# Kernel tuning notes

Measured on AMD Instinct MI355X. Metric: run time of the kernel, lower is better.

The kernel has to match this reference:

```python
import jax, jax.numpy as jnp
import numpy as np

FG_THRESH = 0.5  # fg_iou_thresh in RetinaNetLoss.__init__
BG_THRESH = 0.4  # bg_iou_thresh
BELOW_LOW_QUALITY = -1
BETWEEN_THRESHOLDS = -2


def _make_boxes(key, lead_shape, img_size=800.0, max_wh=128.0):
    # Build valid xyxy boxes (x1<x2, y1<y2) inside an img_size image.
    k1, k2 = jax.random.split(key)
    cxcy = jax.random.uniform(k1, lead_shape + (2,), minval=0.0, maxval=img_size)
    wh = jax.random.uniform(k2, lead_shape + (2,), minval=8.0, maxval=max_wh)
    return jnp.concatenate([cxcy - wh * 0.5, cxcy + wh * 0.5], axis=-1)


def setup_inputs() -> dict:
    key = jax.random.key(0)
    kb, ka = jax.random.split(key)
    B, G, A = 8, 64, 120000
    gt_boxes = _make_boxes(kb, (B, G))                 # [B, G, 4] per-image gt boxes
    anchors = _make_boxes(ka, (A,), max_wh=256.0)      # [A, 4] shared anchors
    return {"gt_boxes": gt_boxes, "anchors": anchors}


def _box_iou(boxes1, boxes2):
    # boxes1 [G,4], boxes2 [A,4] -> IoU [G,A] (torchvision box_ops.box_iou)
    area1 = (boxes1[:, 2] - boxes1[:, 0]) * (boxes1[:, 3] - boxes1[:, 1])  # [G]
    area2 = (boxes2[:, 2] - boxes2[:, 0]) * (boxes2[:, 3] - boxes2[:, 1])  # [A]
    lt = jnp.maximum(boxes1[:, None, :2], boxes2[None, :, :2])  # [G,A,2]
    rb = jnp.minimum(boxes1[:, None, 2:], boxes2[None, :, 2:])  # [G,A,2]
    wh = jnp.clip(rb - lt, 0.0)
    inter = wh[..., 0] * wh[..., 1]  # [G,A]
    return inter / (area1[:, None] + area2[None, :] - inter)


def _match(quality):
    # torchvision Matcher(0.5, 0.4, allow_low_quality_matches=True) on quality [G,A]
    matched_vals = quality.max(axis=0)                      # [A] best IoU per anchor
    all_matches = jnp.argmax(quality, axis=0)               # [A] pre-threshold matches
    matches = jnp.where(matched_vals < BG_THRESH, BELOW_LOW_QUALITY, all_matches)
    matches = jnp.where((matched_vals >= BG_THRESH) & (matched_vals < FG_THRESH),
                        BETWEEN_THRESHOLDS, matches)
    # low-quality match recovery: anchors achieving the per-gt max keep their match
    highest_per_gt = quality.max(axis=1, keepdims=True)     # [G,1]
    pred_update = (quality == highest_per_gt).any(axis=0)   # [A]
    matches = jnp.where(pred_update, all_matches, matches)
    return matches.astype(jnp.int64), matched_vals


def reference(gt_boxes, anchors):
    # gt_boxes [B,G,4], anchors [A,4] -> matched_idxs [B,A] int64, matched_vals [B,A]
    def per_image(boxes):
        return _match(_box_iou(boxes, anchors))
    matched_idxs, matched_vals = jax.vmap(per_image)(gt_boxes)
    return matched_idxs, matched_vals
```

## Files before the change

### kernel.cpp

```cpp
#include <hip/hip_runtime.h>


static constexpr int G = 64;
static constexpr int NCELL = 256;

__device__ __forceinline__ float opaque(float x) {
    asm volatile("" : "+v"(x));
    return x;
}

__device__ __forceinline__ int vindex(int i) {
    asm volatile("" : "+v"(i));
    return i;
}

__device__ __forceinline__ float box_area(float x1, float y1, float x2, float y2) {
    return opaque(__fmul_rn(__fsub_rn(x2, x1), __fsub_rn(y2, y1)));
}

__device__ __forceinline__ float inter_area(float gx1, float gy1, float gx2, float gy2,
                                            float ax1, float ay1, float ax2, float ay2) {
    float ltx = fmaxf(gx1, ax1);
    float lty = fmaxf(gy1, ay1);
    float rbx = fminf(gx2, ax2);
    float rby = fminf(gy2, ay2);
    float w = fmaxf(__fsub_rn(rbx, ltx), 0.0f);
    float h = fmaxf(__fsub_rn(rby, lty), 0.0f);
    return opaque(__fmul_rn(w, h));
}

__device__ __forceinline__ float div_rn(float n, float d) {
    float r = __builtin_amdgcn_rcpf(d);
    float e = fmaf(-d, r, 1.0f);
    r = fmaf(e, r, r);
    float q = __fmul_rn(n, r);
    float s = fmaf(-d, q, n);
    q = fmaf(s, r, q);
    s = fmaf(-d, q, n);
    q = fmaf(s, r, q);
    return q;
}

#define DPP_MAX_STAGE(x, ctrl)                                                   \
    do {                                                                         \
        int _yi = __builtin_amdgcn_update_dpp(__float_as_int(x),                 \
                                              __float_as_int(x), (ctrl),         \
                                              0xf, 0xf, false);                  \
        (x) = fmaxf((x), __int_as_float(_yi));                                   \
    } while (0)

#define DPP_MIN_STAGE(x, ctrl)                                                   \
    do {                                                                         \
        int _yi = __builtin_amdgcn_update_dpp(__float_as_int(x),                 \
                                              __float_as_int(x), (ctrl),         \
                                              0xf, 0xf, false);                  \
        (x) = fminf((x), __int_as_float(_yi));                                   \
    } while (0)

__device__ __forceinline__ float wave_max_lane63(float x) {
    DPP_MAX_STAGE(x, 0xB1);
    DPP_MAX_STAGE(x, 0x4E);
    DPP_MAX_STAGE(x, 0x141);
    DPP_MAX_STAGE(x, 0x140);
    DPP_MAX_STAGE(x, 0x142);
    DPP_MAX_STAGE(x, 0x143);
    return x;
}

__device__ __forceinline__ float wave_min_lane63(float x) {
    DPP_MIN_STAGE(x, 0xB1);
    DPP_MIN_STAGE(x, 0x4E);
    DPP_MIN_STAGE(x, 0x141);
    DPP_MIN_STAGE(x, 0x140);
    DPP_MIN_STAGE(x, 0x142);
    DPP_MIN_STAGE(x, 0x143);
    return x;
}

__device__ __forceinline__ float lane63_bcast(float x) {
    return __int_as_float(__builtin_amdgcn_readlane(__float_as_int(x), 63));
}

__device__ __forceinline__ int cell_of(float4 ab) {
    float cx = (ab.x + ab.z) * 0.5f;
    float cy = (ab.y + ab.w) * 0.5f;
    int cxi = (int)(cx * 0.02f); cxi = cxi < 0 ? 0 : (cxi > 15 ? 15 : cxi);
    int cyi = (int)(cy * 0.02f); cyi = cyi < 0 ? 0 : (cyi > 15 ? 15 : cyi);
    return cyi * 16 + cxi;
}

__global__ void k_count(const float* __restrict__ gt,
                        const float* __restrict__ anchors,
                        unsigned int* __restrict__ bh,
                        unsigned int* __restrict__ hpg,
                        float* __restrict__ gab,
                        int A, int NB, int BG) {
    int t = threadIdx.x;
    int gi = blockIdx.x * 256 + t;
    if (gi < BG) {
        hpg[gi] = 0u;
        float4 gb = ((const float4*)gt)[gi];
        gab[gi] = box_area(gb.x, gb.y, gb.z, gb.w);
    }
    __shared__ unsigned int h[NCELL];
    h[t] = 0u;
    __syncthreads();
    int a = blockIdx.x * 256 + t;
    if (a < A) atomicAdd(&h[cell_of(((const float4*)anchors)[a])], 1u);
    __syncthreads();
    bh[(size_t)t * NB + blockIdx.x] = h[t];
}

__global__ void k_rowscan(unsigned int* __restrict__ bh,
                          unsigned int* __restrict__ cellTot, int NB) {
    const int c = blockIdx.x;
    unsigned int* row = bh + (size_t)c * NB;
    __shared__ unsigned int s[256];
    __shared__ unsigned int carry;
    if (threadIdx.x == 0) carry = 0u;
    __syncthreads();
    for (int base = 0; base < NB; base += 256) {
        int i = base + threadIdx.x;
        unsigned int v = (i < NB) ? row[i] : 0u;
        s[threadIdx.x] = v;
        __syncthreads();
        for (int d = 1; d < 256; d <<= 1) {
            unsigned int add = (threadIdx.x >= d) ? s[threadIdx.x - d] : 0u;
            __syncthreads();
            s[threadIdx.x] += add;
            __syncthreads();
        }
        unsigned int excl = s[threadIdx.x] - v + carry;
        if (i < NB) row[i] = excl;
        __syncthreads();
        if (threadIdx.x == 255) carry += s[255];
        __syncthreads();
    }
    if (threadIdx.x == 0) cellTot[c] = carry;
}

__global__ void k_scat(const float* __restrict__ anchors,
                       const unsigned int* __restrict__ bh,
                       const unsigned int* __restrict__ cellTot,
                       float* __restrict__ sortedA,
                       int* __restrict__ orig, int A, int NB) {
    __shared__ unsigned int cb[NCELL];
    __shared__ unsigned int tot[NCELL];
    __shared__ unsigned int h[NCELL];
    int t = threadIdx.x;
    unsigned int v = cellTot[t];
    cb[t] = v;
    tot[t] = v;
    h[t] = 0u;
    __syncthreads();
    for (int d = 1; d < NCELL; d <<= 1) {
        unsigned int add = (t >= d) ? cb[t - d] : 0u;
        __syncthreads();
        cb[t] += add;
        __syncthreads();
    }
    int a = blockIdx.x * 256 + t;
    if (a < A) {
        float4 ab = ((const float4*)anchors)[a];
        int c = cell_of(ab);
        unsigned int lr = atomicAdd(&h[c], 1u);
        unsigned int base = cb[c] - tot[c];
        unsigned int pos = base + bh[(size_t)c * NB + blockIdx.x] + lr;
        ((float4*)sortedA)[pos] = ab;
        orig[pos] = a;
    }
}

template <bool SCATTER>
__global__ __launch_bounds__(256, 4)
void pass1_k(const float* __restrict__ gt,
             const float* __restrict__ anchors,
             const float* __restrict__ gab,
             unsigned int* __restrict__ hpg,
             unsigned int* __restrict__ sredg,
             int* __restrict__ amaxS,
             const int* __restrict__ orig,
             float2* __restrict__ outiv,
             int A, int nchunks) {
    const int b = blockIdx.y;
    const int t = threadIdx.x;

    __shared__ unsigned int sred[G];
    if (t < G) sred[t] = 0u;
    __syncthreads();

    const int base = blockIdx.x * 1024;
    float ax1[4], ay1[4], ax2[4], ay2[4], aar[4];
    bool val[4];
#pragma unroll
    for (int k = 0; k < 4; ++k) {
        int a = base + k * 256 + t;
        val[k] = (a < A);
        float4 ab = ((const float4*)anchors)[val[k] ? a : 0];
        ax1[k] = val[k] ? ab.x : 3.0e38f;
        ay1[k] = val[k] ? ab.y : 3.0e38f;
        ax2[k] = val[k] ? ab.z : -3.0e38f;
        ay2[k] = val[k] ? ab.w : -3.0e38f;
        aar[k] = val[k] ? box_area(ax1[k], ay1[k], ax2[k], ay2[k]) : 0.0f;
    }

    float wx1 = fminf(fminf(ax1[0], ax1[1]), fminf(ax1[2], ax1[3]));
    float wy1 = fminf(fminf(ay1[0], ay1[1]), fminf(ay1[2], ay1[3]));
    float wx2 = fmaxf(fmaxf(ax2[0], ax2[1]), fmaxf(ax2[2], ax2[3]));
    float wy2 = fmaxf(fmaxf(ay2[0], ay2[1]), fmaxf(ay2[2], ay2[3]));
    wx1 = lane63_bcast(wave_min_lane63(wx1));
    wy1 = lane63_bcast(wave_min_lane63(wy1));
    wx2 = lane63_bcast(wave_max_lane63(wx2));
    wy2 = lane63_bcast(wave_max_lane63(wy2));

    const float4* gtb = (const float4*)gt + (size_t)b * G;
    const float* gas = gab + b * G;

    float vmax[4] = {0.0f, 0.0f, 0.0f, 0.0f};
    int amax[4] = {0, 0, 0, 0};

#pragma unroll 4
    for (int g = 0; g < G; ++g) {
        const int gv = vindex(g);
        const float4 gb = gtb[gv];
        float tlx = fmaxf(gb.x, wx1), trx = fminf(gb.z, wx2);
        float tly = fmaxf(gb.y, wy1), tby = fminf(gb.w, wy2);
        if ((trx > tlx) && (tby > tly)) {
            float inter[4];
#pragma unroll
            for (int k = 0; k < 4; ++k)
                inter[k] = inter_area(gb.x, gb.y, gb.z, gb.w,
                                      ax1[k], ay1[k], ax2[k], ay2[k]);
            float itest = fmaxf(fmaxf(inter[0], inter[1]),
                                fmaxf(inter[2], inter[3]));
            if (__any(itest > 0.0f)) {
                const float ga = gas[gv];
                float m = 0.0f;
#pragma unroll
                for (int k = 0; k < 4; ++k) {
                    float denom = __fsub_rn(__fadd_rn(ga, aar[k]), inter[k]);
                    float q = div_rn(inter[k], denom);
                    if (q > vmax[k]) { vmax[k] = q; amax[k] = g; }
                    m = fmaxf(m, q);
                }
                m = wave_max_lane63(m);
                if ((t & 63) == 63)
                    atomicMax(&sred[g], __float_as_uint(m));
            }
        }
    }

#pragma unroll
    for (int k = 0; k < 4; ++k) {
        if (!val[k]) continue;
        int a = base + k * 256 + t;
        size_t sidx = (size_t)b * A + a;
        amaxS[sidx] = amax[k];
        int mt;
        if (vmax[k] < 0.4f) mt = -1;
        else if (vmax[k] < 0.5f) mt = -2;
        else mt = amax[k];
        int ao = SCATTER ? orig[a] : a;
        outiv[(size_t)b * A + ao] = make_float2((float)mt, vmax[k]);
    }

    __syncthreads();
    if (t < G) {
        atomicMax(&hpg[b * G + t], sred[t]);
        sredg[(size_t)(b * nchunks + blockIdx.x) * G + t] = sred[t];
    }
}

template <bool SCATTER>
__global__ __launch_bounds__(256, 8)
void k_patch(const float* __restrict__ gt,
             const float* __restrict__ anchors,
             const float* __restrict__ gab,
             const unsigned int* __restrict__ hpg,
             const unsigned int* __restrict__ sredg,
             const int* __restrict__ amaxS,
             const int* __restrict__ orig,
             float2* __restrict__ outiv,
             int A, int nchunks) {
    const int b = blockIdx.y;
    const int t = threadIdx.x;
    const int base = blockIdx.x * 1024;

    const unsigned int* sb = sredg + (size_t)(b * nchunks + blockIdx.x) * G;
    const unsigned int* hb = hpg + b * G;

    unsigned long long E = 0ull;
#pragma unroll 16
    for (int g = 0; g < G; ++g)
        E |= (sb[g] == hb[g]) ? (1ull << g) : 0ull;
    if (E == 0ull) return;

    const float4* gtb = (const float4*)gt + (size_t)b * G;
    const float* gas = gab + b * G;
    float ax1[4], ay1[4], ax2[4], ay2[4], aar[4];
    bool val[4];
#pragma unroll
    for (int k = 0; k < 4; ++k) {
        int a = base + k * 256 + t;
        val[k] = (a < A);
        float4 ab = ((const float4*)anchors)[val[k] ? a : 0];
        ax1[k] = val[k] ? ab.x : 3.0e38f;
        ay1[k] = val[k] ? ab.y : 3.0e38f;
        ax2[k] = val[k] ? ab.z : -3.0e38f;
        ay2[k] = val[k] ? ab.w : -3.0e38f;
        aar[k] = val[k] ? box_area(ax1[k], ay1[k], ax2[k], ay2[k]) : 0.0f;
    }

    bool pu[4] = {false, false, false, false};
    unsigned long long e = E;
    while (e) {
        int g = __builtin_ctzll(e);
        e &= e - 1;
        float4 gb = gtb[g];
        float ga = gas[g];
        float hgf = __uint_as_float(hb[g]);
#pragma unroll
        for (int k = 0; k < 4; ++k) {
            float inter = inter_area(gb.x, gb.y, gb.z, gb.w,
                                     ax1[k], ay1[k], ax2[k], ay2[k]);
            float denom = __fsub_rn(__fadd_rn(ga, aar[k]), inter);
            float q = div_rn(inter, denom);
            pu[k] = pu[k] | (q == hgf);
        }
    }

#pragma unroll
    for (int k = 0; k < 4; ++k) {
        int a = base + k * 256 + t;
        if (!val[k] || !pu[k]) continue;
        int ao = SCATTER ? orig[a] : a;
        outiv[(size_t)b * A + ao].x = (float)amaxS[(size_t)b * A + a];
    }
}

__global__ __launch_bounds__(256, 8)
void k_emit(const float2* __restrict__ outiv,
            float* __restrict__ out_idx,
            float* __restrict__ out_val,
            int A) {
    const int b = blockIdx.y;
    const int base = blockIdx.x * 1024;
#pragma unroll
    for (int k = 0; k < 4; ++k) {
        int a = base + k * 256 + threadIdx.x;
        if (a >= A) continue;
        size_t i = (size_t)b * A + a;
        float2 v = outiv[i];
        out_idx[i] = v.x;
        out_val[i] = v.y;
    }
}

extern "C" void kernel_launch(void* const* d_in, const int* in_sizes, int n_in,
                              void* d_out, int out_size, void* d_ws, size_t ws_size,
                              hipStream_t stream) {
    const float* gt = (const float*)d_in[0];
    const float* anchors = (const float*)d_in[1];
    const int BG = in_sizes[0] / 4;
    const int B = BG / G;
    const int A = in_sizes[1] / 4;

    const int nchunks = (A + 1023) / 1024;
    const int NB = (A + 255) / 256;

    unsigned int* ws = (unsigned int*)d_ws;
    unsigned int* hpg = ws;
    float* gab = (float*)(ws + 512);
    unsigned int* cellTot = ws + 1024;
    unsigned int* bh = ws + 1280;
    size_t soff = 1280 + (size_t)NB * 256;
    soff = (soff + 3) & ~(size_t)3;
    float* sortedA = (float*)(ws + soff);
    int* orig = (int*)(ws + soff + 4 * (size_t)A);
    unsigned int* sredg = ws + soff + 5 * (size_t)A;
    size_t ooff = soff + 5 * (size_t)A + (size_t)nchunks * B * G;
    ooff = (ooff + 1) & ~(size_t)1;
    float2* outiv = (float2*)(ws + ooff);
    int* amaxS = (int*)(ws + ooff + 2 * (size_t)B * A);
    const size_t need = (ooff + 3 * (size_t)B * A) * 4;
    const bool sorted = (ws_size >= need);

    float* out_idx = (float*)d_out;
    float* out_val = out_idx + (size_t)B * A;

    dim3 g1(nchunks, B);
    if (sorted) {
        k_count<<<NB, 256, 0, stream>>>(gt, anchors, bh, hpg, gab, A, NB, BG);
        k_rowscan<<<NCELL, 256, 0, stream>>>(bh, cellTot, NB);
        k_scat<<<NB, 256, 0, stream>>>(anchors, bh, cellTot, sortedA, orig, A, NB);
        pass1_k<true><<<g1, 256, 0, stream>>>(gt, sortedA, gab, hpg, sredg,
                                              amaxS, orig, outiv, A, nchunks);
        k_patch<true><<<g1, 256, 0, stream>>>(gt, sortedA, gab, hpg, sredg,
                                              amaxS, orig, outiv, A, nchunks);
        k_emit<<<g1, 256, 0, stream>>>(outiv, out_idx, out_val, A);
    } else {
        k_count<<<NB, 256, 0, stream>>>(gt, anchors, bh, hpg, gab, A, NB, BG);
        pass1_k<false><<<g1, 256, 0, stream>>>(gt, anchors, gab, hpg, sredg,
                                               amaxS, orig, outiv, A, nchunks);
        k_patch<false><<<g1, 256, 0, stream>>>(gt, anchors, gab, hpg, sredg,
                                               amaxS, orig, outiv, A, nchunks);
        k_emit<<<g1, 256, 0, stream>>>(outiv, out_idx, out_val, A);
    }
}
```

Baseline: 67.81 us.

## Process all images per anchor thread and store intermediates anchor-major

The first pass now gives each thread one anchor and loops over all eight images' GT boxes, instead of four anchors per thread for a single image. This reuses anchor loads and wave bounding windows across images and uses 256-anchor chunks, so the GT-window culling is finer. The intermediate outiv/amaxS buffers become anchor-major [A,B], and the patch and emit kernels are reindexed to match. Risks are less per-thread ILP, a longer serial loop per thread, and strided writes in the patch kernel. B is also hardcoded to 8.

New measurement: 135.2 us. +99.3%, slower.

```diff
diff --git a/kernel.cpp b/kernel.cpp
--- a/kernel.cpp
+++ b/kernel.cpp
@@ -2,6 +2,7 @@
 
 
 static constexpr int G = 64;
+static constexpr int B = 8;
 static constexpr int NCELL = 256;
 
 __device__ __forceinline__ float opaque(float x) {
@@ -181,94 +182,80 @@
              int* __restrict__ amaxS,
              const int* __restrict__ orig,
              float2* __restrict__ outiv,
-             int A, int nchunks) {
-    const int b = blockIdx.y;
+             int A) {
     const int t = threadIdx.x;
 
-    __shared__ unsigned int sred[G];
-    if (t < G) sred[t] = 0u;
-    __syncthreads();
-
-    const int base = blockIdx.x * 1024;
-    float ax1[4], ay1[4], ax2[4], ay2[4], aar[4];
-    bool val[4];
+    __shared__ unsigned int sred[B * G];
+    sred[t] = 0u;
+    sred[t + 256] = 0u;
+    __syncthreads();
+
+    const int a = blockIdx.x * 256 + t;
+    const bool v = (a < A);
+    float4 ab = ((const float4*)anchors)[v ? a : 0];
+    float ax1 = v ? ab.x : 3.0e38f;
+    float ay1 = v ? ab.y : 3.0e38f;
+    float ax2 = v ? ab.z : -3.0e38f;
+    float ay2 = v ? ab.w : -3.0e38f;
+    float aar = v ? box_area(ax1, ay1, ax2, ay2) : 0.0f;
+
+    float wx1 = lane63_bcast(wave_min_lane63(ax1));
+    float wy1 = lane63_bcast(wave_min_lane63(ay1));
+    float wx2 = lane63_bcast(wave_max_lane63(ax2));
+    float wy2 = lane63_bcast(wave_max_lane63(ay2));
+
+    const float4* gtb = (const float4*)gt;
+    const float* gas = gab;
+
+    float vmax[B];
+    int amax[B];
 #pragma unroll
-    for (int k = 0; k < 4; ++k) {
-        int a = base + k * 256 + t;
-        val[k] = (a < A);
-        float4 ab = ((const float4*)anchors)[val[k] ? a : 0];
-        ax1[k] = val[k] ? ab.x : 3.0e38f;
-        ay1[k] = val[k] ? ab.y : 3.0e38f;
-        ax2[k] = val[k] ? ab.z : -3.0e38f;
-        ay2[k] = val[k] ? ab.w : -3.0e38f;
-        aar[k] = val[k] ? box_area(ax1[k], ay1[k], ax2[k], ay2[k]) : 0.0f;
-    }
-
-    float wx1 = fminf(fminf(ax1[0], ax1[1]), fminf(ax1[2], ax1[3]));
-    float wy1 = fminf(fminf(ay1[0], ay1[1]), fminf(ay1[2], ay1[3]));
-    float wx2 = fmaxf(fmaxf(ax2[0], ax2[1]), fmaxf(ax2[2], ax2[3]));
-    float wy2 = fmaxf(fmaxf(ay2[0], ay2[1]), fmaxf(ay2[2], ay2[3]));
-    wx1 = lane63_bcast(wave_min_lane63(wx1));
-    wy1 = lane63_bcast(wave_min_lane63(wy1));
-    wx2 = lane63_bcast(wave_max_lane63(wx2));
-    wy2 = lane63_bcast(wave_max_lane63(wy2));
-
-    const float4* gtb = (const float4*)gt + (size_t)b * G;
-    const float* gas = gab + b * G;
-
-    float vmax[4] = {0.0f, 0.0f, 0.0f, 0.0f};
-    int amax[4] = {0, 0, 0, 0};
-
+    for (int b = 0; b < B; ++b) { vmax[b] = 0.0f; amax[b] = 0; }
+
+#pragma unroll
+    for (int b = 0; b < B; ++b) {
 #pragma unroll 4
-    for (int g = 0; g < G; ++g) {
-        const int gv = vindex(g);
-        const float4 gb = gtb[gv];
-        float tlx = fmaxf(gb.x, wx1), trx = fminf(gb.z, wx2);
-        float tly = fmaxf(gb.y, wy1), tby = fminf(gb.w, wy2);
-        if ((trx > tlx) && (tby > tly)) {
-            float inter[4];
-#pragma unroll
-            for (int k = 0; k < 4; ++k)
-                inter[k] = inter_area(gb.x, gb.y, gb.z, gb.w,
-                                      ax1[k], ay1[k], ax2[k], ay2[k]);
-            float itest = fmaxf(fmaxf(inter[0], inter[1]),
-                                fmaxf(inter[2], inter[3]));
-            if (__any(itest > 0.0f)) {
-                const float ga = gas[gv];
-                float m = 0.0f;
-#pragma unroll
-                for (int k = 0; k < 4; ++k) {
-                    float denom = __fsub_rn(__fadd_rn(ga, aar[k]), inter[k]);
-                    float q = div_rn(inter[k], denom);
-                    if (q > vmax[k]) { vmax[k] = q; amax[k] = g; }
-                    m = fmaxf(m, q);
+        for (int g = 0; g < G; ++g) {
+            const int gv = vindex(b * G + g);
+            const float4 gb = gtb[gv];
+            float tlx = fmaxf(gb.x, wx1), trx = fminf(gb.z, wx2);
+            float tly = fmaxf(gb.y, wy1), tby = fminf(gb.w, wy2);
+            if ((trx > tlx) && (tby > tly)) {
+                float inter = inter_area(gb.x, gb.y, gb.z, gb.w,
+                                         ax1, ay1, ax2, ay2);
+                if (__any(inter > 0.0f)) {
+                    const float ga = gas[gv];
+                    float denom = __fsub_rn(__fadd_rn(ga, aar), inter);
+                    float q = div_rn(inter, denom);
+                    if (q > vmax[b]) { vmax[b] = q; amax[b] = g; }
+                    float m = wave_max_lane63(q);
+                    if ((t & 63) == 63)
+                        atomicMax(&sred[b * G + g], __float_as_uint(m));
                 }
-                m = wave_max_lane63(m);
-                if ((t & 63) == 63)
-                    atomicMax(&sred[g], __float_as_uint(m));
             }
         }
     }
 
+    if (v) {
+        int ao = SCATTER ? orig[a] : a;
+        float2* ov = outiv + (size_t)ao * B;
+        int* am = amaxS + (size_t)a * B;
 #pragma unroll
-    for (int k = 0; k < 4; ++k) {
-        if (!val[k]) continue;
-        int a = base + k * 256 + t;
-        size_t sidx = (size_t)b * A + a;
-        amaxS[sidx] = amax[k];
-        int mt;
-        if (vmax[k] < 0.4f) mt = -1;
-        else if (vmax[k] < 0.5f) mt = -2;
-        else mt = amax[k];
-        int ao = SCATTER ? orig[a] : a;
-        outiv[(size_t)b * A + ao] = make_float2((float)mt, vmax[k]);
-    }
-
-    __syncthreads();
-    if (t < G) {
-        atomicMax(&hpg[b * G + t], sred[t]);
-        sredg[(size_t)(b * nchunks + blockIdx.x) * G + t] = sred[t];
-    }
+        for (int b = 0; b < B; ++b) {
+            am[b] = amax[b];
+            int mt;
+            if (vmax[b] < 0.4f) mt = -1;
+            else if (vmax[b] < 0.5f) mt = -2;
+            else mt = amax[b];
+            ov[b] = make_float2((float)mt, vmax[b]);
+        }
+    }
+
+    __syncthreads();
+    atomicMax(&hpg[t], sred[t]);
+    atomicMax(&hpg[t + 256], sred[t + 256]);
+    sredg[(size_t)blockIdx.x * 512 + t] = sred[t];
+    sredg[(size_t)blockIdx.x * 512 + t + 256] = sred[t + 256];
 }
 
 template <bool SCATTER>
@@ -281,12 +268,11 @@
              const int* __restrict__ amaxS,
              const int* __restrict__ orig,
              float2* __restrict__ outiv,
-             int A, int nchunks) {
+             int A) {
     const int b = blockIdx.y;
     const int t = threadIdx.x;
-    const int base = blockIdx.x * 1024;
-
-    const unsigned int* sb = sredg + (size_t)(b * nchunks + blockIdx.x) * G;
+
+    const unsigned int* sb = sredg + (size_t)blockIdx.x * 512 + b * G;
     const unsigned int* hb = hpg + b * G;
 
     unsigned long long E = 0ull;
@@ -295,23 +281,19 @@
         E |= (sb[g] == hb[g]) ? (1ull << g) : 0ull;
     if (E == 0ull) return;
 
+    const int a = blockIdx.x * 256 + t;
+    const bool v = (a < A);
+    float4 ab = ((const float4*)anchors)[v ? a : 0];
+    float ax1 = v ? ab.x : 3.0e38f;
+    float ay1 = v ? ab.y : 3.0e38f;
+    float ax2 = v ? ab.z : -3.0e38f;
+    float ay2 = v ? ab.w : -3.0e38f;
+    float aar = v ? box_area(ax1, ay1, ax2, ay2) : 0.0f;
+
     const float4* gtb = (const float4*)gt + (size_t)b * G;
     const float* gas = gab + b * G;
-    float ax1[4], ay1[4], ax2[4], ay2[4], aar[4];
-    bool val[4];
-#pragma unroll
-    for (int k = 0; k < 4; ++k) {
-        int a = base + k * 256 + t;
-        val[k] = (a < A);
-        float4 ab = ((const float4*)anchors)[val[k] ? a : 0];
-        ax1[k] = val[k] ? ab.x : 3.0e38f;
-        ay1[k] = val[k] ? ab.y : 3.0e38f;
-        ax2[k] = val[k] ? ab.z : -3.0e38f;
-        ay2[k] = val[k] ? ab.w : -3.0e38f;
-        aar[k] = val[k] ? box_area(ax1[k], ay1[k], ax2[k], ay2[k]) : 0.0f;
-    }
-
-    bool pu[4] = {false, false, false, false};
+
+    bool pu = false;
     unsigned long long e = E;
     while (e) {
         int g = __builtin_ctzll(e);
@@ -319,22 +301,15 @@
         float4 gb = gtb[g];
         float ga = gas[g];
         float hgf = __uint_as_float(hb[g]);
-#pragma unroll
-        for (int k = 0; k < 4; ++k) {
-            float inter = inter_area(gb.x, gb.y, gb.z, gb.w,
-                                     ax1[k], ay1[k], ax2[k], ay2[k]);
-            float denom = __fsub_rn(__fadd_rn(ga, aar[k]), inter);
-            float q = div_rn(inter, denom);
-            pu[k] = pu[k] | (q == hgf);
-        }
-    }
-
-#pragma unroll
-    for (int k = 0; k < 4; ++k) {
-        int a = base + k * 256 + t;
-        if (!val[k] || !pu[k]) continue;
+        float inter = inter_area(gb.x, gb.y, gb.z, gb.w, ax1, ay1, ax2, ay2);
+        float denom = __fsub_rn(__fadd_rn(ga, aar), inter);
+        float q = div_rn(inter, denom);
+        pu = pu | (q == hgf);
+    }
+
+    if (v && pu) {
         int ao = SCATTER ? orig[a] : a;
-        outiv[(size_t)b * A + ao].x = (float)amaxS[(size_t)b * A + a];
+        outiv[(size_t)ao * B + b].x = (float)amaxS[(size_t)a * B + b];
     }
 }
 
@@ -343,16 +318,14 @@
             float* __restrict__ out_idx,
             float* __restrict__ out_val,
             int A) {
-    const int b = blockIdx.y;
-    const int base = blockIdx.x * 1024;
+    int a = blockIdx.x * 256 + threadIdx.x;
+    if (a >= A) return;
+    const float2* ov = outiv + (size_t)a * B;
 #pragma unroll
-    for (int k = 0; k < 4; ++k) {
-        int a = base + k * 256 + threadIdx.x;
-        if (a >= A) continue;
-        size_t i = (size_t)b * A + a;
-        float2 v = outiv[i];
-        out_idx[i] = v.x;
-        out_val[i] = v.y;
+    for (int b = 0; b < B; ++b) {
+        float2 vv = ov[b];
+        out_idx[(size_t)b * A + a] = vv.x;
+        out_val[(size_t)b * A + a] = vv.y;
     }
 }
 
@@ -362,10 +335,8 @@
     const float* gt = (const float*)d_in[0];
     const float* anchors = (const float*)d_in[1];
     const int BG = in_sizes[0] / 4;
-    const int B = BG / G;
     const int A = in_sizes[1] / 4;
 
-    const int nchunks = (A + 1023) / 1024;
     const int NB = (A + 255) / 256;
 
     unsigned int* ws = (unsigned int*)d_ws;
@@ -378,8 +349,8 @@
     float* sortedA = (float*)(ws + soff);
     int* orig = (int*)(ws + soff + 4 * (size_t)A);
     unsigned int* sredg = ws + soff + 5 * (size_t)A;
-    size_t ooff = soff + 5 * (size_t)A + (size_t)nchunks * B * G;
-    ooff = (ooff + 1) & ~(size_t)1;
+    size_t ooff = soff + 5 * (size_t)A + (size_t)NB * 512;
+    ooff = (ooff + 15) & ~(size_t)15;
     float2* outiv = (float2*)(ws + ooff);
     int* amaxS = (int*)(ws + ooff + 2 * (size_t)B * A);
     const size_t need = (ooff + 3 * (size_t)B * A) * 4;
@@ -388,22 +359,22 @@
     float* out_idx = (float*)d_out;
     float* out_val = out_idx + (size_t)B * A;
 
-    dim3 g1(nchunks, B);
+    dim3 gp(NB, B);
     if (sorted) {
         k_count<<<NB, 256, 0, stream>>>(gt, anchors, bh, hpg, gab, A, NB, BG);
         k_rowscan<<<NCELL, 256, 0, stream>>>(bh, cellTot, NB);
         k_scat<<<NB, 256, 0, stream>>>(anchors, bh, cellTot, sortedA, orig, A, NB);
-        pass1_k<true><<<g1, 256, 0, stream>>>(gt, sortedA, gab, hpg, sredg,
-                                              amaxS, orig, outiv, A, nchunks);
-        k_patch<true><<<g1, 256, 0, stream>>>(gt, sortedA, gab, hpg, sredg,
-                                              amaxS, orig, outiv, A, nchunks);
-        k_emit<<<g1, 256, 0, stream>>>(outiv, out_idx, out_val, A);
+        pass1_k<true><<<NB, 256, 0, stream>>>(gt, sortedA, gab, hpg, sredg,
+                                              amaxS, orig, outiv, A);
+        k_patch<true><<<gp, 256, 0, stream>>>(gt, sortedA, gab, hpg, sredg,
+                                              amaxS, orig, outiv, A);
+        k_emit<<<NB, 256, 0, stream>>>(outiv, out_idx, out_val, A);
     } else {
         k_count<<<NB, 256, 0, stream>>>(gt, anchors, bh, hpg, gab, A, NB, BG);
-        pass1_k<false><<<g1, 256, 0, stream>>>(gt, anchors, gab, hpg, sredg,
-                                               amaxS, orig, outiv, A, nchunks);
-        k_patch<false><<<g1, 256, 0, stream>>>(gt, anchors, gab, hpg, sredg,
-                                               amaxS, orig, outiv, A, nchunks);
-        k_emit<<<g1, 256, 0, stream>>>(outiv, out_idx, out_val, A);
-    }
-}
+        pass1_k<false><<<NB, 256, 0, stream>>>(gt, anchors, gab, hpg, sredg,
+                                               amaxS, orig, outiv, A);
+        k_patch<false><<<gp, 256, 0, stream>>>(gt, anchors, gab, hpg, sredg,
+                                               amaxS, orig, outiv, A);
+        k_emit<<<NB, 256, 0, stream>>>(outiv, out_idx, out_val, A);
+    }
+}
```
